# Kernel tuning notes

Measured on AMD Instinct MI355X. Metric: run time of the kernel, lower is better.

The kernel has to match this reference:

```python
import jax, jax.numpy as jnp
import numpy as np

N_EMBED = 1024
N_HEAD = 64  # head (value) dimension, per source: Linear(n_embed, n_head)
B = 8
C = 2048


def setup_inputs() -> dict:
    key = jax.random.key(0)
    k1, k2, k3, k4, k5 = jax.random.split(key, 5)
    bound = 1.0 / np.sqrt(N_EMBED)  # torch Linear default init range
    x = jax.random.normal(k1, (B, C, N_EMBED), dtype=jnp.float32)
    Wq = jax.random.uniform(k2, (N_EMBED, N_HEAD), dtype=jnp.float32, minval=-bound, maxval=bound)
    Wk = jax.random.uniform(k3, (N_EMBED, N_HEAD), dtype=jnp.float32, minval=-bound, maxval=bound)
    Wv = jax.random.uniform(k4, (N_EMBED, N_HEAD), dtype=jnp.float32, minval=-bound, maxval=bound)
    zero_mask = jax.random.randint(k5, (B, C), 0, 2) == 1
    return {"x": x, "Wq": Wq, "Wk": Wk, "Wv": Wv, "zero_mask": zero_mask}


def reference(x, Wq, Wk, Wv, zero_mask):
    # x: [B, C, n_embed]; zero_mask: [B, C] bool (zeroes whole query rows post-softmax)
    Bc, Cc, _ = x.shape
    q = x @ Wq  # [B, C, H]
    k = x @ Wk
    v = x @ Wv
    # NOTE: source scales by C**-0.5 (sequence length), not head_dim**-0.5
    scores = jnp.einsum('bqh,bkh->bqk', q, k) * (float(Cc) ** -0.5)  # [B, C, C]
    causal = jnp.tril(jnp.ones((Cc, Cc), dtype=bool))
    scores = jnp.where(causal[None], scores, -jnp.inf)
    a = jax.nn.softmax(scores, axis=-1)
    a = jnp.where(zero_mask[..., None], jnp.zeros((), dtype=a.dtype), a)  # post-softmax zero mask
    return a @ v  # [B, C, H]
```

## Files before the change

kernel.cpp:

```cpp
#include <hip/hip_runtime.h>
#include <math.h>


#define B_ 8
#define C_ 2048
#define E_ 1024
#define H_ 64
#define SCALE 0.02209708691207961f

typedef __attribute__((ext_vector_type(8))) short short8;
typedef __attribute__((ext_vector_type(4))) float floatx4;

union BF8 { short8 s8; unsigned int u[4]; };

static __device__ __forceinline__ unsigned int pack_bf2(float lo, float hi) {
    unsigned int a = __builtin_bit_cast(unsigned int, lo);
    unsigned int b = __builtin_bit_cast(unsigned int, hi);
    return (a >> 16) | (b & 0xFFFF0000u);
}
static __device__ __forceinline__ unsigned short f2bf(float f) {
    return (unsigned short)(__builtin_bit_cast(unsigned int, f) >> 16);
}
static __device__ __forceinline__ void load_lds16(const void* g, void* l) {
    __builtin_amdgcn_global_load_lds(
        (const __attribute__((address_space(1))) void*)g,
        (__attribute__((address_space(3))) void*)l, 16, 0, 0);
}

__global__ __launch_bounds__(256) void wcvt_kernel(
    const float* __restrict__ Wq, const float* __restrict__ Wk,
    const float* __restrict__ Wv, unsigned short* __restrict__ wt)
{
    __shared__ float lds[64][68];
    const int bid = (int)blockIdx.x;
    const int m = bid >> 4, kt = bid & 15, k0 = kt * 64;
    const float* W = (m == 0) ? Wq : (m == 1) ? Wk : Wv;
    const int t = (int)threadIdx.x;
#pragma unroll
    for (int j = 0; j < 4; j++) {
        int idx4 = j * 256 + t;
        int row = idx4 >> 4, c4 = idx4 & 15;
        float4 v = *(const float4*)(W + (size_t)(k0 + row) * 64 + c4 * 4);
        *(float4*)&lds[row][c4 * 4] = v;
    }
    __syncthreads();
#pragma unroll
    for (int j = 0; j < 2; j++) {
        int g = j * 256 + t;
        int n = g >> 3, kk = (g & 7) * 8;
        unsigned int o[4];
#pragma unroll
        for (int i = 0; i < 4; i++)
            o[i] = pack_bf2(lds[kk + 2 * i][n], lds[kk + 2 * i + 1][n]);
        *(uint4*)(wt + (size_t)(m * 64 + n) * 1024 + k0 + kk) =
            make_uint4(o[0], o[1], o[2], o[3]);
    }
}

__global__ __launch_bounds__(256, 2) void qkv_kernel(
    const float* __restrict__ X, const unsigned short* __restrict__ wt,
    unsigned short* __restrict__ qg, unsigned short* __restrict__ kg,
    unsigned short* __restrict__ vtile)
{
    __shared__ unsigned short wlds[2][192 * 64];
    __shared__ unsigned short vstage[64 * 40];

    const int t = (int)threadIdx.x;
    const int w = t >> 6, lane = t & 63;
    const int l15 = lane & 15, quad = lane >> 4;
    const int r0 = (int)blockIdx.x * 32;
    const int mrow = r0 + (w >> 1) * 16 + l15;
    const int ncol0 = (w & 1) * 96;

    const int srow_off = lane >> 3;
    const int sgs = lane & 7;

    floatx4 acc[6];
#pragma unroll
    for (int j = 0; j < 6; j++) acc[j] = (floatx4){0.f, 0.f, 0.f, 0.f};

#pragma unroll
    for (int j = 0; j < 6; j++) {
        const int region = w * 6 + j;
        const int row = region * 8 + srow_off;
        const int gsrc = sgs ^ (row & 7);
        load_lds16(wt + (size_t)row * 1024 + gsrc * 8, &wlds[0][region * 512]);
    }
    float4 xr[4];
#pragma unroll
    for (int kc = 0; kc < 2; kc++) {
        const float* xp = X + (size_t)mrow * E_ + kc * 32 + quad * 8;
        xr[kc * 2]     = *(const float4*)xp;
        xr[kc * 2 + 1] = *(const float4*)(xp + 4);
    }

    int buf = 0;
    for (int c = 0; c < 16; c++) {
        __syncthreads();
        float4 xr2[4];
        if (c < 15) {
            const int k0n = (c + 1) * 64;
#pragma unroll
            for (int kc = 0; kc < 2; kc++) {
                const float* xp = X + (size_t)mrow * E_ + k0n + kc * 32 + quad * 8;
                xr2[kc * 2]     = *(const float4*)xp;
                xr2[kc * 2 + 1] = *(const float4*)(xp + 4);
            }
#pragma unroll
            for (int j = 0; j < 6; j++) {
                const int region = w * 6 + j;
                const int row = region * 8 + srow_off;
                const int gsrc = sgs ^ (row & 7);
                load_lds16(wt + (size_t)row * 1024 + k0n + gsrc * 8,
                           &wlds[buf ^ 1][region * 512]);
            }
        }
#pragma unroll
        for (int kc = 0; kc < 2; kc++) {
            BF8 a;
            float4 f0 = xr[kc * 2], f1 = xr[kc * 2 + 1];
            a.u[0] = pack_bf2(f0.x, f0.y);
            a.u[1] = pack_bf2(f0.z, f0.w);
            a.u[2] = pack_bf2(f1.x, f1.y);
            a.u[3] = pack_bf2(f1.z, f1.w);
#pragma unroll
            for (int nt = 0; nt < 6; nt++) {
                const int n = ncol0 + nt * 16 + l15;
                const int g = kc * 4 + quad;
                short8 bfr = *(const short8*)&wlds[buf][n * 64 + (g ^ (n & 7)) * 8];
                acc[nt] = __builtin_amdgcn_mfma_f32_16x16x32_bf16(
                    a.s8, bfr, acc[nt], 0, 0, 0);
            }
        }
#pragma unroll
        for (int j = 0; j < 4; j++) xr[j] = xr2[j];
        buf ^= 1;
    }

    const int bb = r0 >> 11;
    const int keybase = r0 & 2047;
    const int rowl0 = (w >> 1) * 16 + quad * 4;
#pragma unroll
    for (int nt = 0; nt < 6; nt++) {
        const int n = ncol0 + nt * 16 + l15;
        if (n < 64) {
#pragma unroll
            for (int r = 0; r < 4; r++)
                qg[(size_t)(r0 + rowl0 + r) * 64 + n] = f2bf(acc[nt][r] * SCALE);
        } else if (n < 128) {
#pragma unroll
            for (int r = 0; r < 4; r++)
                kg[(size_t)(r0 + rowl0 + r) * 64 + (n - 64)] = f2bf(acc[nt][r]);
        } else {
            const int h = n - 128;
            unsigned int p0 = pack_bf2(acc[nt][0], acc[nt][1]);
            unsigned int p1 = pack_bf2(acc[nt][2], acc[nt][3]);
            *(unsigned int*)&vstage[h * 40 + rowl0] = p0;
            *(unsigned int*)&vstage[h * 40 + rowl0 + 2] = p1;
        }
    }
    __syncthreads();
    {
        const int h = t >> 2, part = t & 3;
        uint4 v = *(const uint4*)&vstage[h * 40 + part * 8];
        *(uint4*)(vtile + ((size_t)(bb * 32 + (keybase >> 6)) * 64 + h) * 64
                  + (keybase & 63) + part * 8) = v;
    }
}

__global__ __launch_bounds__(128, 2) void attn_kernel(
    const unsigned short* __restrict__ qg, const unsigned short* __restrict__ kg,
    const unsigned short* __restrict__ vtile, const int* __restrict__ zmask,
    float* __restrict__ opart, float* __restrict__ lpart,
    float* __restrict__ out)
{
    __shared__ unsigned short Klds[2][64 * 64];
    __shared__ unsigned short Vlds[2][64 * 64];
    __shared__ unsigned short Ps[2 * 16 * 88];

    const int t = (int)threadIdx.x;
    const int w = t >> 6, lane = t & 63;
    const int l15 = lane & 15, quad = lane >> 4;
    const int b = (int)blockIdx.x;
    const int qt = (int)blockIdx.y;
    const int z = (int)blockIdx.z;
    const int q0 = qt * 32;
    const int nkt = (q0 >> 6) + 1;
    const int t0 = z * 16;
    const int t1 = (z == 0) ? ((nkt < 16) ? nkt : 16) : nkt;
    if (t0 >= t1) return;

    const int qlo = q0 + w * 16;
    const int myrow = qlo + quad * 4;
    const int srow_off = lane >> 3, sgs = lane & 7;

    short8 qfr[2];
#pragma unroll
    for (int kc = 0; kc < 2; kc++)
        qfr[kc] = *(const short8*)(qg + ((size_t)b * C_ + qlo + l15) * 64
                                   + kc * 32 + quad * 8);

    floatx4 accO[4];
#pragma unroll
    for (int i = 0; i < 4; i++) accO[i] = (floatx4){0.f, 0.f, 0.f, 0.f};
    float lsum[4] = {0.f, 0.f, 0.f, 0.f};

#pragma unroll
    for (int j = 0; j < 4; j++) {
        const int region = w * 4 + j;
        const int row = region * 8 + srow_off;
        const int gsrc = sgs ^ (row & 7);
        load_lds16(kg + ((size_t)b * C_ + t0 * 64 + row) * 64 + gsrc * 8,
                   &Klds[0][region * 512]);
        load_lds16(vtile + (((size_t)b * 32 + t0) * 64 + row) * 64 + gsrc * 8,
                   &Vlds[0][region * 512]);
    }

    int buf = 0;
    for (int kt = t0; kt < t1; kt++) {
        __syncthreads();
        if (kt + 1 < t1) {
            const int k0n = (kt + 1) * 64;
#pragma unroll
            for (int j = 0; j < 4; j++) {
                const int region = w * 4 + j;
                const int row = region * 8 + srow_off;
                const int gsrc = sgs ^ (row & 7);
                load_lds16(kg + ((size_t)b * C_ + k0n + row) * 64 + gsrc * 8,
                           &Klds[buf ^ 1][region * 512]);
                load_lds16(vtile + (((size_t)b * 32 + kt + 1) * 64 + row) * 64 + gsrc * 8,
                           &Vlds[buf ^ 1][region * 512]);
            }
        }

        floatx4 s[4];
#pragma unroll
        for (int nt = 0; nt < 4; nt++) {
            const int row = nt * 16 + l15;
            short8 kf0 = *(const short8*)&Klds[buf][row * 64 + ((quad) ^ (row & 7)) * 8];
            short8 kf1 = *(const short8*)&Klds[buf][row * 64 + ((4 + quad) ^ (row & 7)) * 8];
            floatx4 zz = (floatx4){0.f, 0.f, 0.f, 0.f};
            zz = __builtin_amdgcn_mfma_f32_16x16x32_bf16(qfr[0], kf0, zz, 0, 0, 0);
            s[nt] = __builtin_amdgcn_mfma_f32_16x16x32_bf16(qfr[1], kf1, zz, 0, 0, 0);
        }
        float pr[4][4];
#pragma unroll
        for (int nt = 0; nt < 4; nt++)
#pragma unroll
            for (int r = 0; r < 4; r++) pr[nt][r] = __expf(s[nt][r]);
        if (kt == nkt - 1) {
            const int k0 = kt * 64;
#pragma unroll
            for (int nt = 0; nt < 4; nt++) {
                const int key = k0 + nt * 16 + l15;
#pragma unroll
                for (int r = 0; r < 4; r++)
                    if (key > myrow + r) pr[nt][r] = 0.f;
            }
        }
#pragma unroll
        for (int nt = 0; nt < 4; nt++)
#pragma unroll
            for (int r = 0; r < 4; r++) {
                lsum[r] += pr[nt][r];
                Ps[(w * 16 + quad * 4 + r) * 88 + nt * 16 + l15] = f2bf(pr[nt][r]);
            }
#pragma unroll
        for (int kc = 0; kc < 2; kc++) {
            short8 af = *(const short8*)&Ps[(w * 16 + l15) * 88 + kc * 32 + quad * 8];
#pragma unroll
            for (int nt = 0; nt < 4; nt++) {
                const int row = nt * 16 + l15;
                short8 vf = *(const short8*)&Vlds[buf][row * 64
                                + ((kc * 4 + quad) ^ (row & 7)) * 8];
                accO[nt] = __builtin_amdgcn_mfma_f32_16x16x32_bf16(
                    af, vf, accO[nt], 0, 0, 0);
            }
        }
        buf ^= 1;
    }

#pragma unroll
    for (int r = 0; r < 4; r++) {
        float v = lsum[r];
        v += __shfl_xor(v, 1);
        v += __shfl_xor(v, 2);
        v += __shfl_xor(v, 4);
        v += __shfl_xor(v, 8);
        lsum[r] = v;
    }

    if (q0 < 1024) {
        float inv[4];
#pragma unroll
        for (int r = 0; r < 4; r++) {
            int zm = zmask[b * C_ + myrow + r];
            inv[r] = zm ? 0.f : 1.0f / lsum[r];
        }
#pragma unroll
        for (int nt = 0; nt < 4; nt++)
#pragma unroll
            for (int r = 0; r < 4; r++)
                out[(size_t)(b * C_ + myrow + r) * 64 + nt * 16 + l15] =
                    accO[nt][r] * inv[r];
    } else {
        const int lrow = myrow - 1024;
        float* ob = opart + ((size_t)(z * 8 + b) * 1024 + lrow) * 64;
#pragma unroll
        for (int nt = 0; nt < 4; nt++)
#pragma unroll
            for (int r = 0; r < 4; r++)
                ob[(size_t)r * 64 + nt * 16 + l15] = accO[nt][r];
        if (l15 == 0) {
#pragma unroll
            for (int r = 0; r < 4; r++)
                lpart[(size_t)(z * 8 + b) * 1024 + lrow + r] = lsum[r];
        }
    }
}

__global__ __launch_bounds__(256) void combine_kernel(
    const float* __restrict__ opart, const float* __restrict__ lpart,
    const int* __restrict__ zmask, float* __restrict__ out)
{
    const int gid = (int)blockIdx.x * 256 + (int)threadIdx.x;
    const int b = gid >> 14;
    const int rem = gid & 16383;
    const int lrow = rem >> 4;
    const int f4 = rem & 15;

    const size_t o0 = ((size_t)(0 * 8 + b) * 1024 + lrow) * 64 + f4 * 4;
    const size_t o1 = ((size_t)(1 * 8 + b) * 1024 + lrow) * 64 + f4 * 4;
    float4 a = *(const float4*)(opart + o0);
    float4 c = *(const float4*)(opart + o1);
    float l = lpart[(size_t)(0 * 8 + b) * 1024 + lrow]
            + lpart[(size_t)(1 * 8 + b) * 1024 + lrow];
    const int row = 1024 + lrow;
    const float inv = zmask[b * C_ + row] ? 0.f : 1.0f / l;
    *(float4*)(out + (size_t)(b * C_ + row) * 64 + f4 * 4) =
        make_float4((a.x + c.x) * inv, (a.y + c.y) * inv,
                    (a.z + c.z) * inv, (a.w + c.w) * inv);
}

extern "C" void kernel_launch(void* const* d_in, const int* in_sizes, int n_in,
                              void* d_out, int out_size, void* d_ws, size_t ws_size,
                              hipStream_t stream) {
    const float* X  = (const float*)d_in[0];
    const float* Wq = (const float*)d_in[1];
    const float* Wk = (const float*)d_in[2];
    const float* Wv = (const float*)d_in[3];
    const int*   zm = (const int*)d_in[4];
    float* out = (float*)d_out;

    unsigned short* qg    = (unsigned short*)d_ws;
    unsigned short* kg    = qg    + (size_t)B_ * C_ * H_;
    unsigned short* vtile = kg    + (size_t)B_ * C_ * H_;
    unsigned short* wt    = vtile + (size_t)B_ * C_ * H_;
    float* opart = (float*)(wt + (size_t)192 * 1024);
    float* lpart = opart + (size_t)2 * 8 * 1024 * 64;

    wcvt_kernel<<<dim3(48), dim3(256), 0, stream>>>(Wq, Wk, Wv, wt);
    qkv_kernel<<<dim3(512), dim3(256), 0, stream>>>(X, wt, qg, kg, vtile);
    attn_kernel<<<dim3(B_, 64, 2), dim3(128), 0, stream>>>(
        qg, kg, vtile, zm, opart, lpart, out);
    combine_kernel<<<dim3(512), dim3(256), 0, stream>>>(opart, lpart, zm, out);
}
```

Before: 148.0 us.

## Split QKV projection per matrix with full-K weights in LDS; finer attention key split

The QKV projection now runs one block per (128-row tile, Q/K/V matrix). Each block loads that matrix's full 64x1024 bf16 weight slice into padded LDS once, then streams X through a 3-deep register prefetch with no per-chunk barriers. Attention splits keys into chunks of 8 tiles across up to 4 z-slices instead of 2 halves of 16, and the combine kernel sums a variable number of partials for rows 512 and above. This is meant to cut synchronisation in the projection and balance the causal attention work, at the cost of reading X three times, more partial-output traffic, and larger LDS use that limits occupancy.

After: 149.2 us. No clear change (+0.8%).

```diff
diff --git a/kernel.cpp b/kernel.cpp
--- a/kernel.cpp
+++ b/kernel.cpp
@@ -57,114 +57,113 @@
     }
 }
 
-__global__ __launch_bounds__(256, 2) void qkv_kernel(
+__global__ __launch_bounds__(512, 1) void qkv_kernel(
     const float* __restrict__ X, const unsigned short* __restrict__ wt,
     unsigned short* __restrict__ qg, unsigned short* __restrict__ kg,
     unsigned short* __restrict__ vtile)
 {
-    __shared__ unsigned short wlds[2][192 * 64];
-    __shared__ unsigned short vstage[64 * 40];
+    __shared__ unsigned short wlds[64 * 1032];
+    __shared__ unsigned short vstage[64 * 136];
 
     const int t = (int)threadIdx.x;
     const int w = t >> 6, lane = t & 63;
     const int l15 = lane & 15, quad = lane >> 4;
-    const int r0 = (int)blockIdx.x * 32;
-    const int mrow = r0 + (w >> 1) * 16 + l15;
-    const int ncol0 = (w & 1) * 96;
-
-    const int srow_off = lane >> 3;
-    const int sgs = lane & 7;
-
-    floatx4 acc[6];
-#pragma unroll
-    for (int j = 0; j < 6; j++) acc[j] = (floatx4){0.f, 0.f, 0.f, 0.f};
-
-#pragma unroll
-    for (int j = 0; j < 6; j++) {
-        const int region = w * 6 + j;
-        const int row = region * 8 + srow_off;
-        const int gsrc = sgs ^ (row & 7);
-        load_lds16(wt + (size_t)row * 1024 + gsrc * 8, &wlds[0][region * 512]);
-    }
-    float4 xr[4];
-#pragma unroll
-    for (int kc = 0; kc < 2; kc++) {
-        const float* xp = X + (size_t)mrow * E_ + kc * 32 + quad * 8;
-        xr[kc * 2]     = *(const float4*)xp;
-        xr[kc * 2 + 1] = *(const float4*)(xp + 4);
-    }
-
-    int buf = 0;
+    const int rt = (int)blockIdx.x, m = (int)blockIdx.y;
+    const int r0 = rt * 128;
+    const int mrow = r0 + w * 16 + l15;
+    const unsigned short* wsrc = wt + (size_t)m * 64 * 1024;
+
+#pragma unroll
+    for (int j = 0; j < 16; j++) {
+        int idx = j * 512 + t;
+        int row = idx >> 7, g = idx & 127;
+        uint4 v = *(const uint4*)(wsrc + (size_t)row * 1024 + g * 8);
+        *(uint4*)&wlds[row * 1032 + g * 8] = v;
+    }
+
+    floatx4 acc[4];
+#pragma unroll
+    for (int j = 0; j < 4; j++) acc[j] = (floatx4){0.f, 0.f, 0.f, 0.f};
+
+    float4 xb[3][4];
+#pragma unroll
+    for (int p = 0; p < 2; p++)
+#pragma unroll
+        for (int kc = 0; kc < 2; kc++) {
+            const float* xp = X + (size_t)mrow * E_ + p * 64 + kc * 32 + quad * 8;
+            xb[p][kc * 2]     = *(const float4*)xp;
+            xb[p][kc * 2 + 1] = *(const float4*)(xp + 4);
+        }
+
+    __syncthreads();
+
+#pragma unroll
     for (int c = 0; c < 16; c++) {
-        __syncthreads();
-        float4 xr2[4];
-        if (c < 15) {
-            const int k0n = (c + 1) * 64;
+        const int cur = c % 3, nxt = (c + 2) % 3;
+        if (c + 2 < 16) {
+            const int k0n = (c + 2) * 64;
 #pragma unroll
             for (int kc = 0; kc < 2; kc++) {
                 const float* xp = X + (size_t)mrow * E_ + k0n + kc * 32 + quad * 8;
-                xr2[kc * 2]     = *(const float4*)xp;
-                xr2[kc * 2 + 1] = *(const float4*)(xp + 4);
-            }
-#pragma unroll
-            for (int j = 0; j < 6; j++) {
-                const int region = w * 6 + j;
-                const int row = region * 8 + srow_off;
-                const int gsrc = sgs ^ (row & 7);
-                load_lds16(wt + (size_t)row * 1024 + k0n + gsrc * 8,
-                           &wlds[buf ^ 1][region * 512]);
-            }
-        }
-#pragma unroll
-        for (int kc = 0; kc < 2; kc++) {
+                xb[nxt][kc * 2]     = *(const float4*)xp;
+                xb[nxt][kc * 2 + 1] = *(const float4*)(xp + 4);
+            }
+        }
+#pragma unroll
+        for (int ks = 0; ks < 2; ks++) {
             BF8 a;
-            float4 f0 = xr[kc * 2], f1 = xr[kc * 2 + 1];
+            float4 f0 = xb[cur][ks * 2], f1 = xb[cur][ks * 2 + 1];
             a.u[0] = pack_bf2(f0.x, f0.y);
             a.u[1] = pack_bf2(f0.z, f0.w);
             a.u[2] = pack_bf2(f1.x, f1.y);
             a.u[3] = pack_bf2(f1.z, f1.w);
 #pragma unroll
-            for (int nt = 0; nt < 6; nt++) {
-                const int n = ncol0 + nt * 16 + l15;
-                const int g = kc * 4 + quad;
-                short8 bfr = *(const short8*)&wlds[buf][n * 64 + (g ^ (n & 7)) * 8];
+            for (int nt = 0; nt < 4; nt++) {
+                const int n = nt * 16 + l15;
+                short8 bfr = *(const short8*)&wlds[n * 1032 + c * 64
+                                                  + ks * 32 + quad * 8];
                 acc[nt] = __builtin_amdgcn_mfma_f32_16x16x32_bf16(
                     a.s8, bfr, acc[nt], 0, 0, 0);
             }
         }
-#pragma unroll
-        for (int j = 0; j < 4; j++) xr[j] = xr2[j];
-        buf ^= 1;
     }
 
     const int bb = r0 >> 11;
     const int keybase = r0 & 2047;
-    const int rowl0 = (w >> 1) * 16 + quad * 4;
-#pragma unroll
-    for (int nt = 0; nt < 6; nt++) {
-        const int n = ncol0 + nt * 16 + l15;
-        if (n < 64) {
-#pragma unroll
-            for (int r = 0; r < 4; r++)
-                qg[(size_t)(r0 + rowl0 + r) * 64 + n] = f2bf(acc[nt][r] * SCALE);
-        } else if (n < 128) {
-#pragma unroll
-            for (int r = 0; r < 4; r++)
-                kg[(size_t)(r0 + rowl0 + r) * 64 + (n - 64)] = f2bf(acc[nt][r]);
-        } else {
-            const int h = n - 128;
-            unsigned int p0 = pack_bf2(acc[nt][0], acc[nt][1]);
-            unsigned int p1 = pack_bf2(acc[nt][2], acc[nt][3]);
-            *(unsigned int*)&vstage[h * 40 + rowl0] = p0;
-            *(unsigned int*)&vstage[h * 40 + rowl0 + 2] = p1;
-        }
-    }
-    __syncthreads();
-    {
-        const int h = t >> 2, part = t & 3;
-        uint4 v = *(const uint4*)&vstage[h * 40 + part * 8];
-        *(uint4*)(vtile + ((size_t)(bb * 32 + (keybase >> 6)) * 64 + h) * 64
-                  + (keybase & 63) + part * 8) = v;
+    const int rowl = w * 16 + quad * 4;
+    if (m == 0) {
+#pragma unroll
+        for (int nt = 0; nt < 4; nt++)
+#pragma unroll
+            for (int r = 0; r < 4; r++)
+                qg[(size_t)(r0 + rowl + r) * 64 + nt * 16 + l15] =
+                    f2bf(acc[nt][r] * SCALE);
+    } else if (m == 1) {
+#pragma unroll
+        for (int nt = 0; nt < 4; nt++)
+#pragma unroll
+            for (int r = 0; r < 4; r++)
+                kg[(size_t)(r0 + rowl + r) * 64 + nt * 16 + l15] =
+                    f2bf(acc[nt][r]);
+    } else {
+#pragma unroll
+        for (int nt = 0; nt < 4; nt++) {
+            const int h = nt * 16 + l15;
+            *(unsigned int*)&vstage[h * 136 + rowl] =
+                pack_bf2(acc[nt][0], acc[nt][1]);
+            *(unsigned int*)&vstage[h * 136 + rowl + 2] =
+                pack_bf2(acc[nt][2], acc[nt][3]);
+        }
+        __syncthreads();
+#pragma unroll
+        for (int j = 0; j < 2; j++) {
+            int idx = j * 512 + t;
+            int h = idx >> 4, g = idx & 15;
+            uint4 v = *(const uint4*)&vstage[h * 136 + g * 8];
+            int kb = (keybase >> 6) + (g >> 3);
+            *(uint4*)(vtile + (((size_t)bb * 32 + kb) * 64 + h) * 64
+                      + (g & 7) * 8) = v;
+        }
     }
 }
 
@@ -186,9 +185,10 @@
     const int z = (int)blockIdx.z;
     const int q0 = qt * 32;
     const int nkt = (q0 >> 6) + 1;
-    const int t0 = z * 16;
-    const int t1 = (z == 0) ? ((nkt < 16) ? nkt : 16) : nkt;
+    const int t0 = z * 8;
+    const int t1 = (t0 + 8 < nkt) ? (t0 + 8) : nkt;
     if (t0 >= t1) return;
+    const int ns = (nkt + 7) >> 3;
 
     const int qlo = q0 + w * 16;
     const int myrow = qlo + quad * 4;
@@ -290,7 +290,7 @@
         lsum[r] = v;
     }
 
-    if (q0 < 1024) {
+    if (ns == 1) {
         float inv[4];
 #pragma unroll
         for (int r = 0; r < 4; r++) {
@@ -304,8 +304,8 @@
                 out[(size_t)(b * C_ + myrow + r) * 64 + nt * 16 + l15] =
                     accO[nt][r] * inv[r];
     } else {
-        const int lrow = myrow - 1024;
-        float* ob = opart + ((size_t)(z * 8 + b) * 1024 + lrow) * 64;
+        const int lrow = myrow - 512;
+        float* ob = opart + ((size_t)(z * 8 + b) * 1536 + lrow) * 64;
 #pragma unroll
         for (int nt = 0; nt < 4; nt++)
 #pragma unroll
@@ -314,7 +314,7 @@
         if (l15 == 0) {
 #pragma unroll
             for (int r = 0; r < 4; r++)
-                lpart[(size_t)(z * 8 + b) * 1024 + lrow + r] = lsum[r];
+                lpart[(size_t)(z * 8 + b) * 1536 + lrow + r] = lsum[r];
         }
     }
 }
@@ -323,23 +323,25 @@
     const float* __restrict__ opart, const float* __restrict__ lpart,
     const int* __restrict__ zmask, float* __restrict__ out)
 {
+    const int b = (int)blockIdx.y;
     const int gid = (int)blockIdx.x * 256 + (int)threadIdx.x;
-    const int b = gid >> 14;
-    const int rem = gid & 16383;
-    const int lrow = rem >> 4;
-    const int f4 = rem & 15;
-
-    const size_t o0 = ((size_t)(0 * 8 + b) * 1024 + lrow) * 64 + f4 * 4;
-    const size_t o1 = ((size_t)(1 * 8 + b) * 1024 + lrow) * 64 + f4 * 4;
-    float4 a = *(const float4*)(opart + o0);
-    float4 c = *(const float4*)(opart + o1);
-    float l = lpart[(size_t)(0 * 8 + b) * 1024 + lrow]
-            + lpart[(size_t)(1 * 8 + b) * 1024 + lrow];
-    const int row = 1024 + lrow;
+    const int lrow = gid >> 4;
+    const int f4 = gid & 15;
+    const int row = 512 + lrow;
+    const int nkt = (row >> 6) + 1;
+    const int ns = (nkt + 7) >> 3;
+
+    float4 o = make_float4(0.f, 0.f, 0.f, 0.f);
+    float l = 0.f;
+    for (int zc = 0; zc < ns; zc++) {
+        float4 p = *(const float4*)(opart
+            + ((size_t)(zc * 8 + b) * 1536 + lrow) * 64 + f4 * 4);
+        o.x += p.x; o.y += p.y; o.z += p.z; o.w += p.w;
+        l += lpart[(size_t)(zc * 8 + b) * 1536 + lrow];
+    }
     const float inv = zmask[b * C_ + row] ? 0.f : 1.0f / l;
     *(float4*)(out + (size_t)(b * C_ + row) * 64 + f4 * 4) =
-        make_float4((a.x + c.x) * inv, (a.y + c.y) * inv,
-                    (a.z + c.z) * inv, (a.w + c.w) * inv);
+        make_float4(o.x * inv, o.y * inv, o.z * inv, o.w * inv);
 }
 
 extern "C" void kernel_launch(void* const* d_in, const int* in_sizes, int n_in,
@@ -357,11 +359,11 @@
     unsigned short* vtile = kg    + (size_t)B_ * C_ * H_;
     unsigned short* wt    = vtile + (size_t)B_ * C_ * H_;
     float* opart = (float*)(wt + (size_t)192 * 1024);
-    float* lpart = opart + (size_t)2 * 8 * 1024 * 64;
+    float* lpart = opart + (size_t)4 * 8 * 1536 * 64;
 
     wcvt_kernel<<<dim3(48), dim3(256), 0, stream>>>(Wq, Wk, Wv, wt);
-    qkv_kernel<<<dim3(512), dim3(256), 0, stream>>>(X, wt, qg, kg, vtile);
-    attn_kernel<<<dim3(B_, 64, 2), dim3(128), 0, stream>>>(
+    qkv_kernel<<<dim3(128, 3), dim3(512), 0, stream>>>(X, wt, qg, kg, vtile);
+    attn_kernel<<<dim3(B_, 64, 4), dim3(128), 0, stream>>>(
         qg, kg, vtile, zm, opart, lpart, out);
-    combine_kernel<<<dim3(512), dim3(256), 0, stream>>>(opart, lpart, zm, out);
-}
+    combine_kernel<<<dim3(96, B_), dim3(256), 0, stream>>>(opart, lpart, zm, out);
+}
```
